# Optimization experiments

Hardware: AMD Instinct MI355X
Metric: run time of the kernel (lower is better)

The kernel has to match this reference:

```python
import jax, jax.numpy as jnp
import numpy as np

B, C, HW = 128, 3, 224
P = 16
D = 256
NH = 8
HD = D // NH
E = 4            # num_experts
K = 2            # top-k
FF = 4 * D
NC = 38
EPS = 1e-5


def _layernorm(x, g, b):
    mu = jnp.mean(x, axis=-1, keepdims=True)
    var = jnp.mean(jnp.square(x - mu), axis=-1, keepdims=True)
    return (x - mu) * jax.lax.rsqrt(var + EPS) * g + b


def setup_inputs() -> dict:
    key = jax.random.key(0)
    ks = jax.random.split(key, 16)
    s = 0.02
    return {
        "x": jax.random.normal(ks[0], (B, C, HW, HW), dtype=jnp.float32),
        "conv_w": jax.random.normal(ks[1], (D, C, P, P), dtype=jnp.float32) * s,
        "conv_b": jnp.zeros((D,), jnp.float32),
        "cls_token": jnp.zeros((1, 1, D), jnp.float32),
        "ln1_g": jnp.ones((D,), jnp.float32),
        "ln1_b": jnp.zeros((D,), jnp.float32),
        "qkv_w": jax.random.normal(ks[2], (3 * D, D), dtype=jnp.float32) * s,
        "qkv_b": jnp.zeros((3 * D,), jnp.float32),
        "out_w": jax.random.normal(ks[3], (D, D), dtype=jnp.float32) * s,
        "out_b": jnp.zeros((D,), jnp.float32),
        "ln2_g": jnp.ones((D,), jnp.float32),
        "ln2_b": jnp.zeros((D,), jnp.float32),
        "router_w": jax.random.normal(ks[4], (E, D), dtype=jnp.float32) * s,
        "router_b": jnp.zeros((E,), jnp.float32),
        "e_w1": jax.random.normal(ks[5], (E, D, FF), dtype=jnp.float32) * s,
        "e_b1": jnp.zeros((E, FF), jnp.float32),
        "e_w2": jax.random.normal(ks[6], (E, FF, D), dtype=jnp.float32) * s,
        "e_b2": jnp.zeros((E, D), jnp.float32),
        "head_w": jax.random.normal(ks[7], (NC, D), dtype=jnp.float32) * s,
        "head_b": jnp.zeros((NC,), jnp.float32),
    }


def reference(x, conv_w, conv_b, cls_token, ln1_g, ln1_b, qkv_w, qkv_b,
              out_w, out_b, ln2_g, ln2_b, router_w, router_b,
              e_w1, e_b1, e_w2, e_b2, head_w, head_b):
    # patch embed: Conv2d(3, D, 16, 16) -> [B, D, 14, 14] -> [B, 196, D]
    h = jax.lax.conv_general_dilated(
        x, conv_w, window_strides=(P, P), padding="VALID",
        dimension_numbers=("NCHW", "OIHW", "NCHW")) + conv_b[None, :, None, None]
    b = h.shape[0]
    tok = h.reshape(b, D, -1).transpose(0, 2, 1)            # [B, 196, D]
    tok = jnp.concatenate([jnp.broadcast_to(cls_token, (b, 1, D)), tok], axis=1)  # [B, 197, D]
    S = tok.shape[1]

    # Multi-head self-attention (pre-norm)
    x2 = _layernorm(tok, ln1_g, ln1_b)
    qkv = x2 @ qkv_w.T + qkv_b                              # [B, S, 3D]
    q, k, v = jnp.split(qkv, 3, axis=-1)
    q = q.reshape(b, S, NH, HD)
    k = k.reshape(b, S, NH, HD)
    v = v.reshape(b, S, NH, HD)
    scores = jnp.einsum("bqhd,bkhd->bhqk", q, k) / np.float32(np.sqrt(HD))
    attn = jax.nn.softmax(scores, axis=-1)
    ao = jnp.einsum("bhqk,bkhd->bqhd", attn, v).reshape(b, S, D)
    ao = ao @ out_w.T + out_b
    tok = tok + ao

    # MoE FFN (pre-norm). NOTE: original code computes top-k routing weights
    # but never multiplies outputs by them — outputs of selected experts are
    # simply summed. We reproduce that faithfully.
    x2 = _layernorm(tok, ln2_g, ln2_b)
    x_flat = x2.reshape(-1, D)                              # [T, D]
    logits = x_flat @ router_w.T + router_b                 # [T, E]
    probs = jax.nn.softmax(logits, axis=-1)
    _topw, topi = jax.lax.top_k(probs, K)                   # topw unused (as in source)
    mask = (topi[..., None] == jnp.arange(E)).any(axis=1)   # [T, E] bool
    out_flat = jnp.zeros_like(x_flat)
    for i in range(E):                                       # fixed small expert count
        hid = jax.nn.gelu(x_flat @ e_w1[i] + e_b1[i], approximate=False)
        out_flat = out_flat + mask[:, i:i + 1].astype(x_flat.dtype) * (hid @ e_w2[i] + e_b2[i])
    tok = tok + out_flat.reshape(b, S, D)

    return tok[:, 0] @ head_w.T + head_b                    # [B, NC]
```

## Files before the change

kernel.cpp:

```cpp
#include <hip/hip_runtime.h>
#include <hip/hip_bf16.h>
#include <math.h>

#define TTOK   25216
#define SEQL   197
#define NBATCH 128
#define DMODEL 256
#define NHEADS 8
#define FFD    1024
#define NEXP   4
#define NCLS   38
#define CONVK  768
#define NPATCH 196
#define CM     25088

typedef unsigned short u16;
typedef unsigned int u32;
using s16x4 = __attribute__((ext_vector_type(4))) short;
using s16x8 = __attribute__((ext_vector_type(8))) short;
using f32x4 = __attribute__((ext_vector_type(4))) float;

__device__ __forceinline__ float b2f(u16 v) {
  union { unsigned u; float f; } x; x.u = (unsigned)v << 16; return x.f;
}
__device__ __forceinline__ u16 f2b(float f) {
  __hip_bfloat16 h = __float2bfloat16(f);
  return *reinterpret_cast<u16*>(&h);
}
__device__ __forceinline__ void gload16(const void* g, void* l) {
  __builtin_amdgcn_global_load_lds(
      (const __attribute__((address_space(1))) void*)g,
      (__attribute__((address_space(3))) void*)l, 16, 0, 0);
}
__device__ __forceinline__ float warp_sum(float v) {
  #pragma unroll
  for (int o = 32; o; o >>= 1) v += __shfl_xor(v, o);
  return v;
}
__device__ __forceinline__ float warp_max(float v) {
  #pragma unroll
  for (int o = 32; o; o >>= 1) v = fmaxf(v, __shfl_xor(v, o));
  return v;
}
__device__ __forceinline__ int fsw(int row) { return (row ^ (row >> 2)) & 3; }
__device__ __forceinline__ s16x8 ldA72(const u16* base, int rowa, int l4) {
  const char* p = (const char*)base + rowa * 72 + l4 * 16;
  s16x4 a = *(const s16x4*)p;
  s16x4 b = *(const s16x4*)(p + 8);
  return __builtin_shufflevector(a, b, 0, 1, 2, 3, 4, 5, 6, 7);
}

__global__ __launch_bounds__(256) void k_cast2b(const float* __restrict__ cw,
                                                u16* __restrict__ cwh,
                                                u16* __restrict__ cwl,
                                                const float* __restrict__ qw,
                                                u16* __restrict__ qwh,
                                                u16* __restrict__ qwl) {
  int bid = blockIdx.x;
  const float* in = cw; u16* hi = cwh; u16* lo = cwl;
  if (bid >= 192) { bid -= 192; in = qw; hi = qwh; lo = qwl; }
  int i = (bid * 256 + threadIdx.x) * 4;
  float4 v = *(const float4*)&in[i];
  float vv[4] = {v.x, v.y, v.z, v.w};
  u16 h[4], l[4];
  #pragma unroll
  for (int j = 0; j < 4; ++j) {
    h[j] = f2b(vv[j]);
    l[j] = f2b(vv[j] - b2f(h[j]));
  }
  *(uint2*)&hi[i] = *(const uint2*)h;
  *(uint2*)&lo[i] = *(const uint2*)l;
}

__global__ __launch_bounds__(256) void k_conv(const float* __restrict__ x,
                                              const u16* __restrict__ cwh,
                                              const u16* __restrict__ cwl,
                                              const float* __restrict__ cb,
                                              float* __restrict__ tok) {
  const int n0 = blockIdx.x * 128;
  const int m0 = blockIdx.y * 128;
  __shared__ __align__(16) u16 lds[25600];
  u16* Ah_s = lds;
  u16* Al_s = lds + 4608;
  u16* Wbuf = lds + 9216;
  const int tid = threadIdx.x;
  const int lane = tid & 63;
  const int wv = tid >> 6;
  const int wr = wv >> 1, wc = wv & 1;
  const int l15 = lane & 15, l4 = lane >> 4;
  f32x4 acc[4][4] = {};

  const int kpos = (tid & 7) * 4;
  long abase[4]; int aldso[4];
  #pragma unroll
  for (int it = 0; it < 4; ++it) {
    int row = it * 32 + (tid >> 3);
    int m = m0 + row;
    int b = m / NPATCH, p = m - b * NPATCH;
    int py = p / 14, px = p - py * 14;
    abase[it] = (long)(b * 3) * 50176 + (py * 16) * 224 + px * 16;
    aldso[it] = row * 72 + kpos * 2;
  }
  long woff[2]; int wofs[2];
  #pragma unroll
  for (int r = 0; r < 2; ++r) {
    int off = r * 4096 + tid * 16;
    int row = off >> 6;
    int c16 = (off >> 4) & 3;
    int kk = (c16 ^ fsw(row)) << 3;
    woff[r] = (long)(n0 + row) * CONVK + kk;
    wofs[r] = off;
  }
  #pragma unroll
  for (int r = 0; r < 2; ++r) {
    gload16(cwh + woff[r], (char*)Wbuf + wofs[r]);
    gload16(cwl + woff[r], (char*)Wbuf + 8192 + wofs[r]);
  }
  float4 xr[4];
  {
    int c = kpos >> 8, r8 = kpos & 255;
    long soff = (long)c * 50176 + (r8 >> 4) * 224 + (r8 & 15);
    #pragma unroll
    for (int it = 0; it < 4; ++it) xr[it] = *(const float4*)&x[abase[it] + soff];
  }
  int cur = 0;
  for (int kc = 0; kc < CONVK; kc += 32) {
    #pragma unroll
    for (int it = 0; it < 4; ++it) {
      float vv[4] = {xr[it].x, xr[it].y, xr[it].z, xr[it].w};
      u16 h[4], l[4];
      #pragma unroll
      for (int j = 0; j < 4; ++j) {
        h[j] = f2b(vv[j]);
        l[j] = f2b(vv[j] - b2f(h[j]));
      }
      *(uint2*)((char*)Ah_s + aldso[it]) = *(const uint2*)h;
      *(uint2*)((char*)Al_s + aldso[it]) = *(const uint2*)l;
    }
    __syncthreads();
    if (kc + 32 < CONVK) {
      char* wdst = (char*)Wbuf + ((cur ^ 1) << 14);
      #pragma unroll
      for (int r = 0; r < 2; ++r) {
        gload16(cwh + woff[r] + kc + 32, wdst + wofs[r]);
        gload16(cwl + woff[r] + kc + 32, wdst + 8192 + wofs[r]);
      }
      int k = kc + 32 + kpos;
      int c = k >> 8, r8 = k & 255;
      long soff = (long)c * 50176 + (r8 >> 4) * 224 + (r8 & 15);
      #pragma unroll
      for (int it = 0; it < 4; ++it) xr[it] = *(const float4*)&x[abase[it] + soff];
    }
    const char* Wcur = (const char*)Wbuf + (cur << 14);
    s16x8 ah[4], al[4], bh[4], bl[4];
    #pragma unroll
    for (int i = 0; i < 4; ++i) {
      int rowa = wr * 64 + i * 16 + l15;
      ah[i] = ldA72(Ah_s, rowa, l4);
      al[i] = ldA72(Al_s, rowa, l4);
      int rowb = wc * 64 + i * 16 + l15;
      int kbb = (l4 ^ fsw(rowb)) << 4;
      bh[i] = *(const s16x8*)(Wcur + rowb * 64 + kbb);
      bl[i] = *(const s16x8*)(Wcur + 8192 + rowb * 64 + kbb);
    }
    #pragma unroll
    for (int i = 0; i < 4; ++i)
      #pragma unroll
      for (int j = 0; j < 4; ++j)
        acc[i][j] = __builtin_amdgcn_mfma_f32_16x16x32_bf16(ah[i], bh[j],
                                                            acc[i][j], 0, 0, 0);
    #pragma unroll
    for (int i = 0; i < 4; ++i)
      #pragma unroll
      for (int j = 0; j < 4; ++j)
        acc[i][j] = __builtin_amdgcn_mfma_f32_16x16x32_bf16(ah[i], bl[j],
                                                            acc[i][j], 0, 0, 0);
    #pragma unroll
    for (int i = 0; i < 4; ++i)
      #pragma unroll
      for (int j = 0; j < 4; ++j)
        acc[i][j] = __builtin_amdgcn_mfma_f32_16x16x32_bf16(al[i], bh[j],
                                                            acc[i][j], 0, 0, 0);
    __syncthreads();
    cur ^= 1;
  }
  const int mb = m0 + wr * 64 + (l4 << 2);
  const int nb = n0 + wc * 64 + l15;
  #pragma unroll
  for (int i = 0; i < 4; ++i) {
    #pragma unroll
    for (int jf = 0; jf < 4; ++jf) {
      #pragma unroll
      for (int j = 0; j < 4; ++j) {
        int m = mb + i * 16 + j;
        int n = nb + jf * 16;
        int bq = m / NPATCH;
        long cr = (long)bq * SEQL + (m - bq * NPATCH) + 1;
        tok[cr * DMODEL + n] = acc[i][jf][j] + cb[n];
      }
    }
  }
}

__global__ __launch_bounds__(256) void k_lnstat(const float* __restrict__ cls,
                                                float* __restrict__ tok,
                                                float2* __restrict__ st) {
  const int row = blockIdx.x * 4 + (threadIdx.x >> 6);
  const int lane = threadIdx.x & 63;
  const int b = row / SEQL, s = row - b * SEQL;
  float vv[4];
  if (s == 0) {
    *(float4*)vv = *(const float4*)&cls[lane * 4];
    *(float4*)&tok[(size_t)row * DMODEL + lane * 4] = *(const float4*)vv;
  } else {
    *(float4*)vv = *(const float4*)&tok[(size_t)row * DMODEL + lane * 4];
  }
  float s1 = vv[0] + vv[1] + vv[2] + vv[3];
  float s2 = vv[0]*vv[0] + vv[1]*vv[1] + vv[2]*vv[2] + vv[3]*vv[3];
  s1 = warp_sum(s1);
  s2 = warp_sum(s2);
  if (lane == 0) {
    float mu = s1 * (1.f / DMODEL);
    float var = s2 * (1.f / DMODEL) - mu * mu;
    st[row] = make_float2(mu, rsqrtf(var + 1e-5f));
  }
}

__global__ __launch_bounds__(256) void k_qkv(const float* __restrict__ tok,
                                             const float2* __restrict__ stats,
                                             const float* __restrict__ g,
                                             const float* __restrict__ bb,
                                             const u16* __restrict__ Wh,
                                             const u16* __restrict__ Wl,
                                             const float* __restrict__ bias,
                                             float* __restrict__ Cf) {
  const int n0 = blockIdx.x * 128;
  const int m0 = blockIdx.y * 128;
  __shared__ __align__(16) u16 lds[25600];
  u16* Ah_s = lds;
  u16* Al_s = lds + 4608;
  u16* Wbuf = lds + 9216;
  const int tid = threadIdx.x;
  const int lane = tid & 63;
  const int wv = tid >> 6;
  const int wr = wv >> 1, wc = wv & 1;
  const int l15 = lane & 15, l4 = lane >> 4;
  f32x4 acc[4][4] = {};

  const int kpos = (tid & 7) * 4;
  long atok[4]; float2 st[4]; int aldso[4];
  #pragma unroll
  for (int it = 0; it < 4; ++it) {
    int row = it * 32 + (tid >> 3);
    int m = m0 + row;
    atok[it] = (long)m * DMODEL;
    st[it] = stats[m];
    aldso[it] = row * 72 + kpos * 2;
  }
  long woff[2]; int wofs[2];
  #pragma unroll
  for (int r = 0; r < 2; ++r) {
    int off = r * 4096 + tid * 16;
    int row = off >> 6;
    int c16 = (off >> 4) & 3;
    int kk = (c16 ^ fsw(row)) << 3;
    woff[r] = (long)(n0 + row) * DMODEL + kk;
    wofs[r] = off;
  }
  #pragma unroll
  for (int r = 0; r < 2; ++r) {
    gload16(Wh + woff[r], (char*)Wbuf + wofs[r]);
    gload16(Wl + woff[r], (char*)Wbuf + 8192 + wofs[r]);
  }
  float4 xr[4], gr, br;
  #pragma unroll
  for (int it = 0; it < 4; ++it) xr[it] = *(const float4*)&tok[atok[it] + kpos];
  gr = *(const float4*)&g[kpos];
  br = *(const float4*)&bb[kpos];
  int cur = 0;
  for (int kc = 0; kc < DMODEL; kc += 32) {
    float gg[4] = {gr.x, gr.y, gr.z, gr.w};
    float bbv[4] = {br.x, br.y, br.z, br.w};
    #pragma unroll
    for (int it = 0; it < 4; ++it) {
      float vv[4] = {xr[it].x, xr[it].y, xr[it].z, xr[it].w};
      u16 h[4], l[4];
      #pragma unroll
      for (int j = 0; j < 4; ++j) {
        float xd = (vv[j] - st[it].x) * st[it].y * gg[j] + bbv[j];
        h[j] = f2b(xd);
        l[j] = f2b(xd - b2f(h[j]));
      }
      *(uint2*)((char*)Ah_s + aldso[it]) = *(const uint2*)h;
      *(uint2*)((char*)Al_s + aldso[it]) = *(const uint2*)l;
    }
    __syncthreads();
    if (kc + 32 < DMODEL) {
      char* wdst = (char*)Wbuf + ((cur ^ 1) << 14);
      #pragma unroll
      for (int r = 0; r < 2; ++r) {
        gload16(Wh + woff[r] + kc + 32, wdst + wofs[r]);
        gload16(Wl + woff[r] + kc + 32, wdst + 8192 + wofs[r]);
      }
      #pragma unroll
      for (int it = 0; it < 4; ++it)
        xr[it] = *(const float4*)&tok[atok[it] + kc + 32 + kpos];
      gr = *(const float4*)&g[kc + 32 + kpos];
      br = *(const float4*)&bb[kc + 32 + kpos];
    }
    const char* Wcur = (const char*)Wbuf + (cur << 14);
    s16x8 ah[4], al[4], bh[4], bl[4];
    #pragma unroll
    for (int i = 0; i < 4; ++i) {
      int rowa = wr * 64 + i * 16 + l15;
      ah[i] = ldA72(Ah_s, rowa, l4);
      al[i] = ldA72(Al_s, rowa, l4);
      int rowb = wc * 64 + i * 16 + l15;
      int kbb = (l4 ^ fsw(rowb)) << 4;
      bh[i] = *(const s16x8*)(Wcur + rowb * 64 + kbb);
      bl[i] = *(const s16x8*)(Wcur + 8192 + rowb * 64 + kbb);
    }
    #pragma unroll
    for (int i = 0; i < 4; ++i)
      #pragma unroll
      for (int j = 0; j < 4; ++j)
        acc[i][j] = __builtin_amdgcn_mfma_f32_16x16x32_bf16(ah[i], bh[j],
                                                            acc[i][j], 0, 0, 0);
    #pragma unroll
    for (int i = 0; i < 4; ++i)
      #pragma unroll
      for (int j = 0; j < 4; ++j)
        acc[i][j] = __builtin_amdgcn_mfma_f32_16x16x32_bf16(ah[i], bl[j],
                                                            acc[i][j], 0, 0, 0);
    #pragma unroll
    for (int i = 0; i < 4; ++i)
      #pragma unroll
      for (int j = 0; j < 4; ++j)
        acc[i][j] = __builtin_amdgcn_mfma_f32_16x16x32_bf16(al[i], bh[j],
                                                            acc[i][j], 0, 0, 0);
    __syncthreads();
    cur ^= 1;
  }
  const int mb = m0 + wr * 64 + (l4 << 2);
  const int nb = n0 + wc * 64 + l15;
  #pragma unroll
  for (int i = 0; i < 4; ++i) {
    #pragma unroll
    for (int jf = 0; jf < 4; ++jf) {
      #pragma unroll
      for (int j = 0; j < 4; ++j) {
        int m = mb + i * 16 + j;
        int n = nb + jf * 16;
        Cf[(long)m * 512 + n] = acc[i][jf][j] + bias[n];
      }
    }
  }
}

__global__ __launch_bounds__(256) void k_qcls1(const float* __restrict__ cls,
                                               const float* __restrict__ g,
                                               const float* __restrict__ bb,
                                               const u16* __restrict__ qwh,
                                               const u16* __restrict__ qwl,
                                               const float* __restrict__ qb,
                                               float* __restrict__ qf) {
  const int n = threadIdx.x, w = n >> 6, lane = n & 63;
  __shared__ float xs[DMODEL];
  __shared__ float red[8];
  float v = cls[n];
  float s1 = warp_sum(v), s2 = warp_sum(v * v);
  if (lane == 0) { red[w] = s1; red[4 + w] = s2; }
  __syncthreads();
  s1 = red[0] + red[1] + red[2] + red[3];
  s2 = red[4] + red[5] + red[6] + red[7];
  float mu = s1 * (1.f / DMODEL);
  float var = s2 * (1.f / DMODEL) - mu * mu;
  float rs = rsqrtf(var + 1e-5f);
  xs[n] = (v - mu) * rs * g[n] + bb[n];
  __syncthreads();
  float val = qb[n];
  #pragma unroll 4
  for (int i = 0; i < 32; ++i) {
    s16x8 wh = *(const s16x8*)(qwh + (size_t)n * DMODEL + i * 8);
    s16x8 wl = *(const s16x8*)(qwl + (size_t)n * DMODEL + i * 8);
    #pragma unroll
    for (int j = 0; j < 8; ++j)
      val = fmaf(b2f((u16)wh[j]) + b2f((u16)wl[j]), xs[i * 8 + j], val);
  }
  qf[n] = val;
}

__global__ __launch_bounds__(256) void k_attn_cls(const float* __restrict__ qf,
                                                  const float* __restrict__ kvf,
                                                  float* __restrict__ ao) {
  const int w = threadIdx.x >> 6, lane = threadIdx.x & 63;
  const int unit = blockIdx.x * 4 + w;
  const int b = unit >> 3, h = unit & 7;
  __shared__ float Ss[4][200];
  float q[32];
  #pragma unroll
  for (int i = 0; i < 8; ++i) {
    float4 q4 = *(const float4*)(qf + h * 32 + i * 4);
    q[i * 4 + 0] = q4.x; q[i * 4 + 1] = q4.y;
    q[i * 4 + 2] = q4.z; q[i * 4 + 3] = q4.w;
  }
  float sc[4];
  float mx = -1e30f;
  #pragma unroll
  for (int r = 0; r < 4; ++r) {
    int k = lane + 64 * r;
    float s = -1e30f;
    if (k < SEQL) {
      const float* kr = kvf + ((size_t)(b * SEQL + k)) * 512 + h * 32;
      s = 0.f;
      #pragma unroll
      for (int i = 0; i < 8; ++i) {
        float4 kv4 = *(const float4*)(kr + i * 4);
        s = fmaf(kv4.x, q[i * 4 + 0], s);
        s = fmaf(kv4.y, q[i * 4 + 1], s);
        s = fmaf(kv4.z, q[i * 4 + 2], s);
        s = fmaf(kv4.w, q[i * 4 + 3], s);
      }
      s *= 0.17677669529663687f;
    }
    sc[r] = s;
    mx = fmaxf(mx, s);
  }
  mx = warp_max(mx);
  float sm = 0.f;
  #pragma unroll
  for (int r = 0; r < 4; ++r) {
    int k = lane + 64 * r;
    float e = (k < SEQL) ? __expf(sc[r] - mx) : 0.f;
    sc[r] = e;
    sm += e;
  }
  sm = warp_sum(sm);
  float inv = 1.f / sm;
  #pragma unroll
  for (int r = 0; r < 4; ++r) {
    int k = lane + 64 * r;
    if (k < SEQL) Ss[w][k] = sc[r] * inv;
  }
  int d = lane & 31, half = lane >> 5;
  float acc = 0.f;
  for (int i = 0; i < 99; ++i) {
    int k = half * 99 + i;
    if (k < SEQL)
      acc = fmaf(Ss[w][k], kvf[((size_t)(b * SEQL + k)) * 512 + 256 + h * 32 + d], acc);
  }
  acc += __shfl_xor(acc, 32);
  if (lane < 32) ao[(b * NHEADS + h) * 32 + d] = acc;
}

__global__ __launch_bounds__(256) void k_oproj_route(
    const float* __restrict__ ao, const float* __restrict__ ow,
    const float* __restrict__ ob, const float* __restrict__ cls,
    const float* __restrict__ g, const float* __restrict__ bb,
    const float* __restrict__ rw, const float* __restrict__ rb,
    float* __restrict__ tokc, float* __restrict__ x2cf,
    float* __restrict__ maskf) {
  const int b = blockIdx.x, n = threadIdx.x;
  const int w = n >> 6, lane = n & 63;
  __shared__ float xs[DMODEL];
  __shared__ float xd_s[DMODEL];
  __shared__ float red[8];
  __shared__ float lg[4];
  xs[n] = ao[b * DMODEL + n];
  __syncthreads();
  float val = ob[n];
  #pragma unroll 4
  for (int i = 0; i < 64; ++i) {
    float4 wv = *(const float4*)(ow + (size_t)n * DMODEL + i * 4);
    val = fmaf(wv.x, xs[i * 4 + 0], val);
    val = fmaf(wv.y, xs[i * 4 + 1], val);
    val = fmaf(wv.z, xs[i * 4 + 2], val);
    val = fmaf(wv.w, xs[i * 4 + 3], val);
  }
  float t = cls[n] + val;
  tokc[b * DMODEL + n] = t;
  float s1 = warp_sum(t), s2 = warp_sum(t * t);
  if (lane == 0) { red[w] = s1; red[4 + w] = s2; }
  __syncthreads();
  s1 = red[0] + red[1] + red[2] + red[3];
  s2 = red[4] + red[5] + red[6] + red[7];
  float mu = s1 * (1.f / DMODEL);
  float var = s2 * (1.f / DMODEL) - mu * mu;
  float rs = rsqrtf(var + 1e-5f);
  float xd = (t - mu) * rs * g[n] + bb[n];
  x2cf[b * DMODEL + n] = xd;
  xd_s[n] = xd;
  __syncthreads();
  float s = 0.f;
  #pragma unroll
  for (int i = 0; i < 4; ++i) s = fmaf(xd_s[lane + i * 64], rw[w * DMODEL + lane + i * 64], s);
  s = warp_sum(s) + rb[w];
  if (lane == 0) lg[w] = s;
  __syncthreads();
  if (n < NEXP) {
    int e = n;
    int rank = 0;
    #pragma unroll
    for (int j = 0; j < NEXP; ++j)
      if (j != e && (lg[j] > lg[e] || (lg[j] == lg[e] && j < e))) ++rank;
    maskf[b * NEXP + e] = (rank < 2) ? 1.f : 0.f;
  }
}

__global__ __launch_bounds__(256) void k_moe1(const float* __restrict__ x2cf,
                                              const float* __restrict__ w1,
                                              const float* __restrict__ b1,
                                              const float* __restrict__ maskf,
                                              float* __restrict__ hid) {
  const int e = blockIdx.x, t = blockIdx.y;
  if (maskf[t * NEXP + e] == 0.f) return;
  __shared__ float xs[DMODEL];
  const int tid = threadIdx.x;
  xs[tid] = x2cf[t * DMODEL + tid];
  __syncthreads();
  const float* w1e = w1 + (size_t)e * DMODEL * FFD + tid;
  float a0 = 0.f, a1 = 0.f, a2 = 0.f, a3 = 0.f;
  #pragma unroll 4
  for (int k = 0; k < DMODEL; ++k) {
    float xv = xs[k];
    const float* wr_ = w1e + (size_t)k * FFD;
    a0 = fmaf(xv, wr_[0], a0);
    a1 = fmaf(xv, wr_[256], a1);
    a2 = fmaf(xv, wr_[512], a2);
    a3 = fmaf(xv, wr_[768], a3);
  }
  float accs[4] = {a0, a1, a2, a3};
  float* hrow = hid + ((size_t)e * NBATCH + t) * FFD;
  #pragma unroll
  for (int j = 0; j < 4; ++j) {
    float v = accs[j] + b1[e * FFD + tid + j * 256];
    hrow[tid + j * 256] = 0.5f * v * (1.0f + erff(v * 0.70710678118654752f));
  }
}

__global__ __launch_bounds__(256) void k_moe2(const float* __restrict__ hid,
                                              const float* __restrict__ w2,
                                              const float* __restrict__ b2,
                                              const float* __restrict__ maskf,
                                              float* __restrict__ tokc) {
  const int t = blockIdx.x, dc = blockIdx.y;
  const int tid = threadIdx.x;
  const int dl = tid & 127, kh = tid >> 7;
  const int dout = dc * 128 + dl;
  int e0 = 0;
  while (e0 < 3 && maskf[t * NEXP + e0] == 0.f) ++e0;
  int e1 = e0 + 1;
  while (e1 < 3 && maskf[t * NEXP + e1] == 0.f) ++e1;
  __shared__ float hs0[FFD], hs1[FFD];
  const float* h0 = hid + ((size_t)e0 * NBATCH + t) * FFD;
  const float* h1 = hid + ((size_t)e1 * NBATCH + t) * FFD;
  for (int i = tid * 4; i < FFD; i += 1024) {
    *(float4*)&hs0[i] = *(const float4*)&h0[i];
    *(float4*)&hs1[i] = *(const float4*)&h1[i];
  }
  __syncthreads();
  const float* w20 = w2 + (size_t)e0 * FFD * DMODEL + dout;
  const float* w21 = w2 + (size_t)e1 * FFD * DMODEL + dout;
  float a0 = 0.f, a1 = 0.f;
  const int k0 = kh * 512;
  #pragma unroll 8
  for (int k = k0; k < k0 + 512; ++k) {
    a0 = fmaf(hs0[k], w20[(size_t)k * DMODEL], a0);
    a1 = fmaf(hs1[k], w21[(size_t)k * DMODEL], a1);
  }
  __shared__ float red[256];
  red[tid] = a0 + a1;
  __syncthreads();
  if (kh == 0) {
    float full = red[dl] + red[128 + dl] +
                 b2[e0 * DMODEL + dout] + b2[e1 * DMODEL + dout];
    tokc[t * DMODEL + dout] += full;
  }
}

__global__ __launch_bounds__(256) void k_head(const float* __restrict__ tokc,
                                              const float* __restrict__ hw,
                                              const float* __restrict__ hb,
                                              float* __restrict__ out) {
  int b = blockIdx.x;
  int w = threadIdx.x >> 6, lane = threadIdx.x & 63;
  const float* row = tokc + (size_t)b * DMODEL;
  for (int c = w; c < NCLS; c += 4) {
    float s = 0.f;
    for (int d = lane; d < DMODEL; d += 64) s = fmaf(row[d], hw[c * DMODEL + d], s);
    s = warp_sum(s);
    if (lane == 0) out[b * NCLS + c] = s + hb[c];
  }
}

extern "C" void kernel_launch(void* const* d_in, const int* in_sizes, int n_in,
                              void* d_out, int out_size, void* d_ws, size_t ws_size,
                              hipStream_t stream) {
  const float* x      = (const float*)d_in[0];
  const float* conv_w = (const float*)d_in[1];
  const float* conv_b = (const float*)d_in[2];
  const float* cls    = (const float*)d_in[3];
  const float* ln1g   = (const float*)d_in[4];
  const float* ln1b   = (const float*)d_in[5];
  const float* qkv_w  = (const float*)d_in[6];
  const float* qkv_b  = (const float*)d_in[7];
  const float* out_w  = (const float*)d_in[8];
  const float* out_b  = (const float*)d_in[9];
  const float* ln2g   = (const float*)d_in[10];
  const float* ln2b   = (const float*)d_in[11];
  const float* rw     = (const float*)d_in[12];
  const float* rb     = (const float*)d_in[13];
  const float* e_w1   = (const float*)d_in[14];
  const float* e_b1   = (const float*)d_in[15];
  const float* e_w2   = (const float*)d_in[16];
  const float* e_b2   = (const float*)d_in[17];
  const float* head_w = (const float*)d_in[18];
  const float* head_b = (const float*)d_in[19];
  float* out = (float*)d_out;

  char* ws = (char*)d_ws;
  size_t off = 0;
  auto alloc = [&](size_t bytes) {
    void* p = ws + off;
    off += (bytes + 255) & ~(size_t)255;
    return p;
  };
  float*  tok   = (float*)alloc((size_t)TTOK * DMODEL * 4);
  float*  qkvf  = (float*)alloc((size_t)TTOK * 512 * 4);
  float2* stats = (float2*)alloc((size_t)TTOK * 8);
  u16*    cwh   = (u16*)alloc((size_t)DMODEL * CONVK * 2);
  u16*    cwl   = (u16*)alloc((size_t)DMODEL * CONVK * 2);
  u16*    qwh   = (u16*)alloc((size_t)768 * DMODEL * 2);
  u16*    qwl   = (u16*)alloc((size_t)768 * DMODEL * 2);
  float*  qf    = (float*)alloc((size_t)DMODEL * 4);
  float*  aocf  = (float*)alloc((size_t)NBATCH * DMODEL * 4);
  float*  tokc  = (float*)alloc((size_t)NBATCH * DMODEL * 4);
  float*  x2cf  = (float*)alloc((size_t)NBATCH * DMODEL * 4);
  float*  maskf = (float*)alloc((size_t)NBATCH * NEXP * 4);
  float*  hid   = (float*)alloc((size_t)NEXP * NBATCH * FFD * 4);

  k_cast2b<<<384, 256, 0, stream>>>(conv_w, cwh, cwl, qkv_w, qwh, qwl);

  k_qcls1<<<1, 256, 0, stream>>>(cls, ln1g, ln1b, qwh, qwl, qkv_b, qf);

  k_conv<<<dim3(2, CM / 128), 256, 0, stream>>>(x, cwh, cwl, conv_b, tok);

  k_lnstat<<<TTOK / 4, 256, 0, stream>>>(cls, tok, stats);

  k_qkv<<<dim3(4, TTOK / 128), 256, 0, stream>>>(
      tok, stats, ln1g, ln1b, qwh + 256 * DMODEL, qwl + 256 * DMODEL,
      qkv_b + 256, qkvf);

  k_attn_cls<<<NBATCH * NHEADS / 4, 256, 0, stream>>>(qf, qkvf, aocf);

  k_oproj_route<<<NBATCH, 256, 0, stream>>>(aocf, out_w, out_b, cls,
                                            ln2g, ln2b, rw, rb,
                                            tokc, x2cf, maskf);

  k_moe1<<<dim3(NEXP, NBATCH), 256, 0, stream>>>(x2cf, e_w1, e_b1, maskf, hid);
  k_moe2<<<dim3(NBATCH, 2), 256, 0, stream>>>(hid, e_w2, e_b2, maskf, tokc);

  k_head<<<NBATCH, 256, 0, stream>>>(tokc, head_w, head_b, out);
}
```

Measured before the change: 207.0 us.

## Double-buffer A tiles in conv and QKV GEMMs to halve barriers

Restructures the conv and QKV GEMM main loops to double-buffer the split-bf16 A tile in LDS alongside the weight tile. The loop is unrolled by two k-steps so each barrier interval both converts and stores the next A tile and runs MFMAs on the current one. This cuts the barriers per k-step from two to one and lets the conversion work overlap with matrix math. In exchange, LDS per block grows from about 50KB to about 68KB and more registers are live (two prefetch register sets), which may lower occupancy.

```diff
diff --git a/kernel.cpp b/kernel.cpp
--- a/kernel.cpp
+++ b/kernel.cpp
@@ -79,10 +79,9 @@
                                               float* __restrict__ tok) {
   const int n0 = blockIdx.x * 128;
   const int m0 = blockIdx.y * 128;
-  __shared__ __align__(16) u16 lds[25600];
-  u16* Ah_s = lds;
-  u16* Al_s = lds + 4608;
-  u16* Wbuf = lds + 9216;
+  __shared__ __align__(16) u16 lds[34816];
+  char* Ab = (char*)lds;
+  char* Wb = (char*)lds + 36864;
   const int tid = threadIdx.x;
   const int lane = tid & 63;
   const int wv = tid >> 6;
@@ -111,79 +110,101 @@
     woff[r] = (long)(n0 + row) * CONVK + kk;
     wofs[r] = off;
   }
-  #pragma unroll
-  for (int r = 0; r < 2; ++r) {
-    gload16(cwh + woff[r], (char*)Wbuf + wofs[r]);
-    gload16(cwl + woff[r], (char*)Wbuf + 8192 + wofs[r]);
-  }
-  float4 xr[4];
-  {
-    int c = kpos >> 8, r8 = kpos & 255;
-    long soff = (long)c * 50176 + (r8 >> 4) * 224 + (r8 & 15);
-    #pragma unroll
-    for (int it = 0; it < 4; ++it) xr[it] = *(const float4*)&x[abase[it] + soff];
-  }
-  int cur = 0;
-  for (int kc = 0; kc < CONVK; kc += 32) {
-    #pragma unroll
-    for (int it = 0; it < 4; ++it) {
-      float vv[4] = {xr[it].x, xr[it].y, xr[it].z, xr[it].w};
-      u16 h[4], l[4];
-      #pragma unroll
-      for (int j = 0; j < 4; ++j) {
-        h[j] = f2b(vv[j]);
-        l[j] = f2b(vv[j] - b2f(h[j]));
-      }
-      *(uint2*)((char*)Ah_s + aldso[it]) = *(const uint2*)h;
-      *(uint2*)((char*)Al_s + aldso[it]) = *(const uint2*)l;
+#define CONV_LOADX(dst, kk_)                                                  \
+  {                                                                           \
+    int k_ = (kk_) + kpos;                                                    \
+    int c_ = k_ >> 8, r8_ = k_ & 255;                                         \
+    long so_ = (long)c_ * 50176 + (r8_ >> 4) * 224 + (r8_ & 15);              \
+    _Pragma("unroll")                                                         \
+    for (int it = 0; it < 4; ++it)                                            \
+      dst[it] = *(const float4*)&x[abase[it] + so_];                          \
+  }
+#define CONV_WRA(src, bufj)                                                   \
+  {                                                                           \
+    char* ah_ = Ab + (bufj) * 18432;                                          \
+    char* al_ = ah_ + 9216;                                                   \
+    _Pragma("unroll")                                                         \
+    for (int it = 0; it < 4; ++it) {                                          \
+      float vv[4] = {src[it].x, src[it].y, src[it].z, src[it].w};             \
+      u16 h_[4], l_[4];                                                       \
+      _Pragma("unroll")                                                       \
+      for (int j = 0; j < 4; ++j) {                                           \
+        h_[j] = f2b(vv[j]);                                                   \
+        l_[j] = f2b(vv[j] - b2f(h_[j]));                                      \
+      }                                                                       \
+      *(uint2*)(ah_ + aldso[it]) = *(const uint2*)h_;                         \
+      *(uint2*)(al_ + aldso[it]) = *(const uint2*)l_;                         \
+    }                                                                         \
+  }
+#define CONV_GLW(kk_, bufj)                                                   \
+  {                                                                           \
+    char* wd_ = Wb + (bufj) * 16384;                                          \
+    _Pragma("unroll")                                                         \
+    for (int r = 0; r < 2; ++r) {                                             \
+      gload16(cwh + woff[r] + (kk_), wd_ + wofs[r]);                          \
+      gload16(cwl + woff[r] + (kk_), wd_ + 8192 + wofs[r]);                   \
+    }                                                                         \
+  }
+#define CONV_MMA(bufj)                                                        \
+  {                                                                           \
+    const u16* ah_ = (const u16*)(Ab + (bufj) * 18432);                       \
+    const u16* al_ = (const u16*)(Ab + (bufj) * 18432 + 9216);                \
+    const char* wc_ = Wb + (bufj) * 16384;                                    \
+    s16x8 ah[4], al[4], bh[4], bl[4];                                         \
+    _Pragma("unroll")                                                         \
+    for (int i = 0; i < 4; ++i) {                                             \
+      int rowa = wr * 64 + i * 16 + l15;                                      \
+      ah[i] = ldA72(ah_, rowa, l4);                                           \
+      al[i] = ldA72(al_, rowa, l4);                                           \
+      int rowb = wc * 64 + i * 16 + l15;                                      \
+      int kbb = (l4 ^ fsw(rowb)) << 4;                                        \
+      bh[i] = *(const s16x8*)(wc_ + rowb * 64 + kbb);                         \
+      bl[i] = *(const s16x8*)(wc_ + 8192 + rowb * 64 + kbb);                  \
+    }                                                                         \
+    _Pragma("unroll")                                                         \
+    for (int i = 0; i < 4; ++i)                                               \
+      _Pragma("unroll")                                                       \
+      for (int j = 0; j < 4; ++j)                                             \
+        acc[i][j] = __builtin_amdgcn_mfma_f32_16x16x32_bf16(ah[i], bh[j],     \
+                                                            acc[i][j], 0, 0, 0); \
+    _Pragma("unroll")                                                         \
+    for (int i = 0; i < 4; ++i)                                               \
+      _Pragma("unroll")                                                       \
+      for (int j = 0; j < 4; ++j)                                             \
+        acc[i][j] = __builtin_amdgcn_mfma_f32_16x16x32_bf16(ah[i], bl[j],     \
+                                                            acc[i][j], 0, 0, 0); \
+    _Pragma("unroll")                                                         \
+    for (int i = 0; i < 4; ++i)                                               \
+      _Pragma("unroll")                                                       \
+      for (int j = 0; j < 4; ++j)                                             \
+        acc[i][j] = __builtin_amdgcn_mfma_f32_16x16x32_bf16(al[i], bh[j],     \
+                                                            acc[i][j], 0, 0, 0); \
+  }
+
+  float4 xr0[4], xr1[4];
+  CONV_GLW(0, 0);
+  CONV_LOADX(xr0, 0);
+  CONV_LOADX(xr1, 32);
+  CONV_WRA(xr0, 0);
+  __syncthreads();
+  for (int kc = 0; kc < CONVK; kc += 64) {
+    CONV_GLW(kc + 32, 1);
+    if (kc + 64 < CONVK) CONV_LOADX(xr0, kc + 64);
+    CONV_WRA(xr1, 1);
+    CONV_MMA(0);
+    __syncthreads();
+    if (kc + 64 < CONVK) {
+      CONV_GLW(kc + 64, 0);
+      if (kc + 96 < CONVK) CONV_LOADX(xr1, kc + 96);
+      CONV_WRA(xr0, 0);
     }
+    CONV_MMA(1);
     __syncthreads();
-    if (kc + 32 < CONVK) {
-      char* wdst = (char*)Wbuf + ((cur ^ 1) << 14);
-      #pragma unroll
-      for (int r = 0; r < 2; ++r) {
-        gload16(cwh + woff[r] + kc + 32, wdst + wofs[r]);
-        gload16(cwl + woff[r] + kc + 32, wdst + 8192 + wofs[r]);
-      }
-      int k = kc + 32 + kpos;
-      int c = k >> 8, r8 = k & 255;
-      long soff = (long)c * 50176 + (r8 >> 4) * 224 + (r8 & 15);
-      #pragma unroll
-      for (int it = 0; it < 4; ++it) xr[it] = *(const float4*)&x[abase[it] + soff];
-    }
-    const char* Wcur = (const char*)Wbuf + (cur << 14);
-    s16x8 ah[4], al[4], bh[4], bl[4];
-    #pragma unroll
-    for (int i = 0; i < 4; ++i) {
-      int rowa = wr * 64 + i * 16 + l15;
-      ah[i] = ldA72(Ah_s, rowa, l4);
-      al[i] = ldA72(Al_s, rowa, l4);
-      int rowb = wc * 64 + i * 16 + l15;
-      int kbb = (l4 ^ fsw(rowb)) << 4;
-      bh[i] = *(const s16x8*)(Wcur + rowb * 64 + kbb);
-      bl[i] = *(const s16x8*)(Wcur + 8192 + rowb * 64 + kbb);
-    }
-    #pragma unroll
-    for (int i = 0; i < 4; ++i)
-      #pragma unroll
-      for (int j = 0; j < 4; ++j)
-        acc[i][j] = __builtin_amdgcn_mfma_f32_16x16x32_bf16(ah[i], bh[j],
-                                                            acc[i][j], 0, 0, 0);
-    #pragma unroll
-    for (int i = 0; i < 4; ++i)
-      #pragma unroll
-      for (int j = 0; j < 4; ++j)
-        acc[i][j] = __builtin_amdgcn_mfma_f32_16x16x32_bf16(ah[i], bl[j],
-                                                            acc[i][j], 0, 0, 0);
-    #pragma unroll
-    for (int i = 0; i < 4; ++i)
-      #pragma unroll
-      for (int j = 0; j < 4; ++j)
-        acc[i][j] = __builtin_amdgcn_mfma_f32_16x16x32_bf16(al[i], bh[j],
-                                                            acc[i][j], 0, 0, 0);
-    __syncthreads();
-    cur ^= 1;
-  }
+  }
+#undef CONV_LOADX
+#undef CONV_WRA
+#undef CONV_GLW
+#undef CONV_MMA
   const int mb = m0 + wr * 64 + (l4 << 2);
   const int nb = n0 + wc * 64 + l15;
   #pragma unroll
@@ -236,10 +257,9 @@
                                              float* __restrict__ Cf) {
   const int n0 = blockIdx.x * 128;
   const int m0 = blockIdx.y * 128;
-  __shared__ __align__(16) u16 lds[25600];
-  u16* Ah_s = lds;
-  u16* Al_s = lds + 4608;
-  u16* Wbuf = lds + 9216;
+  __shared__ __align__(16) u16 lds[34816];
+  char* Ab = (char*)lds;
+  char* Wb = (char*)lds + 36864;
   const int tid = threadIdx.x;
   const int lane = tid & 63;
   const int wv = tid >> 6;
@@ -267,80 +287,104 @@
     woff[r] = (long)(n0 + row) * DMODEL + kk;
     wofs[r] = off;
   }
-  #pragma unroll
-  for (int r = 0; r < 2; ++r) {
-    gload16(Wh + woff[r], (char*)Wbuf + wofs[r]);
-    gload16(Wl + woff[r], (char*)Wbuf + 8192 + wofs[r]);
-  }
-  float4 xr[4], gr, br;
-  #pragma unroll
-  for (int it = 0; it < 4; ++it) xr[it] = *(const float4*)&tok[atok[it] + kpos];
-  gr = *(const float4*)&g[kpos];
-  br = *(const float4*)&bb[kpos];
-  int cur = 0;
-  for (int kc = 0; kc < DMODEL; kc += 32) {
-    float gg[4] = {gr.x, gr.y, gr.z, gr.w};
-    float bbv[4] = {br.x, br.y, br.z, br.w};
-    #pragma unroll
-    for (int it = 0; it < 4; ++it) {
-      float vv[4] = {xr[it].x, xr[it].y, xr[it].z, xr[it].w};
-      u16 h[4], l[4];
-      #pragma unroll
-      for (int j = 0; j < 4; ++j) {
-        float xd = (vv[j] - st[it].x) * st[it].y * gg[j] + bbv[j];
-        h[j] = f2b(xd);
-        l[j] = f2b(xd - b2f(h[j]));
-      }
-      *(uint2*)((char*)Ah_s + aldso[it]) = *(const uint2*)h;
-      *(uint2*)((char*)Al_s + aldso[it]) = *(const uint2*)l;
+#define QKV_LOADX(dst, gdst, bdst, kk_)                                       \
+  {                                                                           \
+    int k_ = (kk_) + kpos;                                                    \
+    _Pragma("unroll")                                                         \
+    for (int it = 0; it < 4; ++it)                                            \
+      dst[it] = *(const float4*)&tok[atok[it] + k_];                          \
+    gdst = *(const float4*)&g[k_];                                            \
+    bdst = *(const float4*)&bb[k_];                                           \
+  }
+#define QKV_WRA(src, gsrc, bsrc, bufj)                                        \
+  {                                                                           \
+    char* ah_ = Ab + (bufj) * 18432;                                          \
+    char* al_ = ah_ + 9216;                                                   \
+    float gg_[4] = {gsrc.x, gsrc.y, gsrc.z, gsrc.w};                          \
+    float bv_[4] = {bsrc.x, bsrc.y, bsrc.z, bsrc.w};                          \
+    _Pragma("unroll")                                                         \
+    for (int it = 0; it < 4; ++it) {                                          \
+      float vv[4] = {src[it].x, src[it].y, src[it].z, src[it].w};             \
+      u16 h_[4], l_[4];                                                       \
+      _Pragma("unroll")                                                       \
+      for (int j = 0; j < 4; ++j) {                                           \
+        float xd_ = (vv[j] - st[it].x) * st[it].y * gg_[j] + bv_[j];          \
+        h_[j] = f2b(xd_);                                                     \
+        l_[j] = f2b(xd_ - b2f(h_[j]));                                        \
+      }                                                                       \
+      *(uint2*)(ah_ + aldso[it]) = *(const uint2*)h_;                         \
+      *(uint2*)(al_ + aldso[it]) = *(const uint2*)l_;                         \
+    }                                                                         \
+  }
+#define QKV_GLW(kk_, bufj)                                                    \
+  {                                                                           \
+    char* wd_ = Wb + (bufj) * 16384;                                          \
+    _Pragma("unroll")                                                         \
+    for (int r = 0; r < 2; ++r) {                                             \
+      gload16(Wh + woff[r] + (kk_), wd_ + wofs[r]);                           \
+      gload16(Wl + woff[r] + (kk_), wd_ + 8192 + wofs[r]);                    \
+    }                                                                         \
+  }
+#define QKV_MMA(bufj)                                                         \
+  {                                                                           \
+    const u16* ah_ = (const u16*)(Ab + (bufj) * 18432);                       \
+    const u16* al_ = (const u16*)(Ab + (bufj) * 18432 + 9216);                \
+    const char* wc_ = Wb + (bufj) * 16384;                                    \
+    s16x8 ah[4], al[4], bh[4], bl[4];                                         \
+    _Pragma("unroll")                                                         \
+    for (int i = 0; i < 4; ++i) {                                             \
+      int rowa = wr * 64 + i * 16 + l15;                                      \
+      ah[i] = ldA72(ah_, rowa, l4);                                           \
+      al[i] = ldA72(al_, rowa, l4);                                           \
+      int rowb = wc * 64 + i * 16 + l15;                                      \
+      int kbb = (l4 ^ fsw(rowb)) << 4;                                        \
+      bh[i] = *(const s16x8*)(wc_ + rowb * 64 + kbb);                         \
+      bl[i] = *(const s16x8*)(wc_ + 8192 + rowb * 64 + kbb);                  \
+    }                                                                         \
+    _Pragma("unroll")                                                         \
+    for (int i = 0; i < 4; ++i)                                               \
+      _Pragma("unroll")                                                       \
+      for (int j = 0; j < 4; ++j)                                             \
+        acc[i][j] = __builtin_amdgcn_mfma_f32_16x16x32_bf16(ah[i], bh[j],     \
+                                                            acc[i][j], 0, 0, 0); \
+    _Pragma("unroll")                                                         \
+    for (int i = 0; i < 4; ++i)                                               \
+      _Pragma("unroll")                                                       \
+      for (int j = 0; j < 4; ++j)                                             \
+        acc[i][j] = __builtin_amdgcn_mfma_f32_16x16x32_bf16(ah[i], bl[j],     \
+                                                            acc[i][j], 0, 0, 0); \
+    _Pragma("unroll")                                                         \
+    for (int i = 0; i < 4; ++i)                                               \
+      _Pragma("unroll")                                                       \
+      for (int j = 0; j < 4; ++j)                                             \
+        acc[i][j] = __builtin_amdgcn_mfma_f32_16x16x32_bf16(al[i], bh[j],     \
+                                                            acc[i][j], 0, 0, 0); \
+  }
+
+  float4 xr0[4], xr1[4], gr0, gr1, br0, br1;
+  QKV_GLW(0, 0);
+  QKV_LOADX(xr0, gr0, br0, 0);
+  QKV_LOADX(xr1, gr1, br1, 32);
+  QKV_WRA(xr0, gr0, br0, 0);
+  __syncthreads();
+  for (int kc = 0; kc < DMODEL; kc += 64) {
+    QKV_GLW(kc + 32, 1);
+    if (kc + 64 < DMODEL) QKV_LOADX(xr0, gr0, br0, kc + 64);
+    QKV_WRA(xr1, gr1, br1, 1);
+    QKV_MMA(0);
+    __syncthreads();
+    if (kc + 64 < DMODEL) {
+      QKV_GLW(kc + 64, 0);
+      if (kc + 96 < DMODEL) QKV_LOADX(xr1, gr1, br1, kc + 96);
+      QKV_WRA(xr0, gr0, br0, 0);
     }
+    QKV_MMA(1);
     __syncthreads();
-    if (kc + 32 < DMODEL) {
-      char* wdst = (char*)Wbuf + ((cur ^ 1) << 14);
-      #pragma unroll
-      for (int r = 0; r < 2; ++r) {
-        gload16(Wh + woff[r] + kc + 32, wdst + wofs[r]);
-        gload16(Wl + woff[r] + kc + 32, wdst + 8192 + wofs[r]);
-      }
-      #pragma unroll
-      for (int it = 0; it < 4; ++it)
-        xr[it] = *(const float4*)&tok[atok[it] + kc + 32 + kpos];
-      gr = *(const float4*)&g[kc + 32 + kpos];
-      br = *(const float4*)&bb[kc + 32 + kpos];
-    }
-    const char* Wcur = (const char*)Wbuf + (cur << 14);
-    s16x8 ah[4], al[4], bh[4], bl[4];
-    #pragma unroll
-    for (int i = 0; i < 4; ++i) {
-      int rowa = wr * 64 + i * 16 + l15;
-      ah[i] = ldA72(Ah_s, rowa, l4);
-      al[i] = ldA72(Al_s, rowa, l4);
-      int rowb = wc * 64 + i * 16 + l15;
-      int kbb = (l4 ^ fsw(rowb)) << 4;
-      bh[i] = *(const s16x8*)(Wcur + rowb * 64 + kbb);
-      bl[i] = *(const s16x8*)(Wcur + 8192 + rowb * 64 + kbb);
-    }
-    #pragma unroll
-    for (int i = 0; i < 4; ++i)
-      #pragma unroll
-      for (int j = 0; j < 4; ++j)
-        acc[i][j] = __builtin_amdgcn_mfma_f32_16x16x32_bf16(ah[i], bh[j],
-                                                            acc[i][j], 0, 0, 0);
-    #pragma unroll
-    for (int i = 0; i < 4; ++i)
-      #pragma unroll
-      for (int j = 0; j < 4; ++j)
-        acc[i][j] = __builtin_amdgcn_mfma_f32_16x16x32_bf16(ah[i], bl[j],
-                                                            acc[i][j], 0, 0, 0);
-    #pragma unroll
-    for (int i = 0; i < 4; ++i)
-      #pragma unroll
-      for (int j = 0; j < 4; ++j)
-        acc[i][j] = __builtin_amdgcn_mfma_f32_16x16x32_bf16(al[i], bh[j],
-                                                            acc[i][j], 0, 0, 0);
-    __syncthreads();
-    cur ^= 1;
-  }
+  }
+#undef QKV_LOADX
+#undef QKV_WRA
+#undef QKV_GLW
+#undef QKV_MMA
   const int mb = m0 + wr * 64 + (l4 << 2);
   const int nb = n0 + wc * 64 + l15;
   #pragma unroll
```

Result: slower. 256.2 us (+23.8%).
